# Performance work log

Hardware: AMD Instinct MI355X
Metric: run time of the kernel (lower is better)

Reference implementation:

```python
import jax, jax.numpy as jnp
import numpy as np

ROLE_BITS = 20
NHEAD = 16
D_MODEL = 1024
D_KEY = D_MODEL // NHEAD  # 64
D_FIL = 512
DFF = 4096
EPS = 1e-5


def _ln(x, g, b):
    mu = jnp.mean(x, axis=-1, keepdims=True)
    var = jnp.mean(jnp.square(x - mu), axis=-1, keepdims=True)
    return (x - mu) * jax.lax.rsqrt(var + EPS) * g + b


def setup_inputs() -> dict:
    key = jax.random.key(0)
    ks = jax.random.split(key, 10)
    N, BSZ, MEM = 16384, 16, 8
    D_IN = D_FIL + ROLE_BITS  # 532
    values = jax.random.normal(ks[0], (N, D_FIL), jnp.float32)
    role_index = jax.random.randint(ks[1], (N,), 1, 2 ** ROLE_BITS)
    # every (batch, memory_slot) pair occupied -> static shapes (compression is a no-op)
    slot = jax.random.permutation(ks[2], jnp.tile(jnp.arange(BSZ * MEM), N // (BSZ * MEM)))
    batch_index = (slot // MEM).astype(jnp.int32)
    memory_index = (slot % MEM).astype(jnp.int32)
    query_vectors = jax.random.normal(ks[3], (NHEAD, D_KEY), jnp.float32) * (1.0 / np.sqrt(D_KEY))
    s = 0.02
    Wk = jax.random.normal(ks[4], (D_MODEL, D_IN), jnp.float32) * s
    Wv = jax.random.normal(ks[5], (D_MODEL, D_IN), jnp.float32) * s
    Wo = jax.random.normal(ks[6], (D_MODEL, D_MODEL), jnp.float32) * s
    W1 = jax.random.normal(ks[7], (DFF, D_MODEL), jnp.float32) * s
    W2 = jax.random.normal(ks[8], (D_MODEL, DFF), jnp.float32) * s
    return dict(
        values=values, role_index=role_index, batch_index=batch_index,
        memory_index=memory_index, query_vectors=query_vectors,
        Wk=Wk, Wv=Wv, Wo=Wo, bo=jnp.zeros((D_MODEL,), jnp.float32),
        W1=W1, b1=jnp.zeros((DFF,), jnp.float32),
        W2=W2, b2=jnp.zeros((D_MODEL,), jnp.float32),
        g_fil=jnp.ones((D_FIL,), jnp.float32), b_fil=jnp.zeros((D_FIL,), jnp.float32),
        g_mha=jnp.ones((D_IN,), jnp.float32), b_mha=jnp.zeros((D_IN,), jnp.float32),
        g_ff=jnp.ones((D_MODEL,), jnp.float32), b_ff=jnp.zeros((D_MODEL,), jnp.float32),
        g_out=jnp.ones((D_MODEL,), jnp.float32), b_out=jnp.zeros((D_MODEL,), jnp.float32),
        bsz=BSZ, memory_slots=MEM,
    )


def _tree_positional_encodings(role_index):
    # bit-expand role indices: column j is bit j of the role index
    bits = (jnp.bitwise_and(role_index[:, None], 2 ** jnp.arange(ROLE_BITS)) != 0).astype(jnp.float32)
    # locate the highest set bit (torch: flip + argmax)
    mi = jnp.argmax(bits[:, ::-1], axis=1)
    cm = ROLE_BITS - 1 - mi  # index of highest set bit
    bits = bits * (1.0 - jax.nn.one_hot(cm, ROLE_BITS, dtype=bits.dtype))  # zero it out
    branch = jnp.arange(ROLE_BITS)[None, :] < cm[:, None]
    return jnp.where(branch, (bits - 0.5) * 2.0, bits)  # {0,1} -> {-1,1} below MSB


def reference(values, role_index, batch_index, memory_index, query_vectors,
              Wk, Wv, Wo, bo, W1, b1, W2, b2,
              g_fil, b_fil, g_mha, b_mha, g_ff, b_ff, g_out, b_out,
              bsz, memory_slots):
    N = values.shape[0]
    T = bsz * memory_slots  # num_trees (all (batch, slot) pairs occupied)

    tpd = _tree_positional_encodings(role_index)
    x = jnp.concatenate([_ln(values, g_fil, b_fil), tpd], axis=1)  # [N, d_input]
    x = _ln(x, g_mha, b_mha)
    k = (x @ Wk.T).reshape(N, NHEAD, D_KEY)
    v = (x @ Wv.T).reshape(N, NHEAD, D_KEY)
    qkm = jnp.einsum('nhd,hd->nh', k, query_vectors)  # [N, H]

    # combined batch+memory mask: node n attends to flat tree t = b*mem + m
    node_slot = batch_index * memory_slots + memory_index  # [N]
    mask = node_slot[:, None] == jnp.arange(T)[None, :]  # [N, T]
    scores = jnp.where(mask[:, :, None], qkm[:, None, :], -1e9) / np.sqrt(D_KEY)
    attn = jax.nn.softmax(scores, axis=0)  # softmax over nodes, [N, T, H]
    out = jnp.einsum('nhv,nth->thv', v, attn).reshape(T, D_MODEL)

    # post-attention: proj_o + residual with flattened queries, LN, FF, LN
    r1 = (out @ Wo.T + bo) + query_vectors.reshape(-1)
    l1 = _ln(r1, g_ff, b_ff)
    ff = jax.nn.gelu(l1 @ W1.T + b1, approximate=False) @ W2.T + b2
    l2 = _ln(ff + r1, g_out, b_out)

    rectangle_out = l2.reshape(bsz, memory_slots, D_MODEL)
    agent_pad_mask = jnp.zeros((bsz, memory_slots), dtype=bool)
    return rectangle_out, agent_pad_mask
```

## Files before the change

kernel.cpp:

```cpp
#include <hip/hip_runtime.h>
#include <hip/hip_bf16.h>

typedef __hip_bfloat16 bf16;

#define N_NODES 16384
#define D_FIL 512
#define D_IN 532
#define D_MODEL 1024
#define NHEAD 16
#define D_KEY 64
#define DFF 4096
#define NTREE 128
#define MEM_SLOTS 8
#define NODES_PER_TREE 128
#define EPS 1e-5f
#define XSE 544
#define XSU 272
#define CSTR 32
#define BSTR 40

typedef float f32x4 __attribute__((ext_vector_type(4)));
typedef short s16x8 __attribute__((ext_vector_type(8)));

union PackU { uint4 u; s16x8 s; };

__device__ inline float gelu_exact(float x) {
    return 0.5f * x * (1.0f + erff(x * 0.7071067811865476f));
}

__device__ inline void blockReduceSum2_512(float& a, float& b, float* sm) {
    int tid = threadIdx.x;
    int lane = tid & 63, wid = tid >> 6;
#pragma unroll
    for (int off = 32; off > 0; off >>= 1) {
        a += __shfl_down(a, off, 64);
        b += __shfl_down(b, off, 64);
    }
    if (lane == 0) { sm[wid] = a; sm[8 + wid] = b; }
    __syncthreads();
    if (tid == 0) {
        float s0 = 0.f, s1 = 0.f;
#pragma unroll
        for (int i = 0; i < 8; ++i) { s0 += sm[i]; s1 += sm[8 + i]; }
        sm[16] = s0; sm[17] = s1;
    }
    __syncthreads();
    a = sm[16]; b = sm[17];
}

__global__ __launch_bounds__(256) void prep_kernel(
        const float* __restrict__ values, const int* __restrict__ role,
        const int* __restrict__ bidx, const int* __restrict__ midx,
        const float* __restrict__ g_fil, const float* __restrict__ b_fil,
        const float* __restrict__ g_mha, const float* __restrict__ b_mha,
        bf16* __restrict__ xs, int* __restrict__ counts,
        const float* __restrict__ q, const float* __restrict__ Wk,
        unsigned* __restrict__ wqb,
        const float* __restrict__ Wv, float* __restrict__ wvt) {
    int b = blockIdx.x;
    int tid = threadIdx.x;

    if (b < 16) {
        int h = b;
        __shared__ float qs[64];
        if (tid < 64) qs[tid] = q[h * 64 + tid];
        __syncthreads();
        for (int p = tid; p < XSU; p += 256) {
            unsigned out = 0u;
            if (p < 266) {
                float a0 = 0.f, a1 = 0.f;
                int j0 = 2 * p;
#pragma unroll 8
                for (int d = 0; d < 64; ++d) {
                    const float* wr = Wk + (size_t)(h * 64 + d) * D_IN;
                    a0 += qs[d] * wr[j0];
                    a1 += qs[d] * wr[j0 + 1];
                }
                unsigned u0 = (unsigned)__bfloat16_as_ushort(__float2bfloat16(a0));
                unsigned u1 = (unsigned)__bfloat16_as_ushort(__float2bfloat16(a1));
                out = (u1 << 16) | u0;
            }
            wqb[h * XSU + p] = out;
        }
        return;
    }

    if (b < 560) {
        __shared__ float tile[32][33];
        int vb = b - 16;
        int c0 = (vb & 31) * 32, j0 = (vb >> 5) * 32;
        int tx = tid & 31, ty = tid >> 5;
#pragma unroll
        for (int r = 0; r < 4; ++r) {
            int cc = ty + r * 8;
            int j = j0 + tx;
            tile[cc][tx] = (j < D_IN) ? Wv[(size_t)(c0 + cc) * D_IN + j] : 0.f;
        }
        __syncthreads();
#pragma unroll
        for (int r = 0; r < 4; ++r) {
            int j = j0 + ty + r * 8;
            if (j < D_IN) wvt[(size_t)j * D_MODEL + c0 + tx] = tile[tx][ty + r * 8];
        }
        return;
    }

    int wave = tid >> 6;
    int l = tid & 63;
    int n = (b - 560) * 4 + wave;

    const float4* vp = (const float4*)(values + (size_t)n * D_FIL + l * 8);
    float4 v0 = vp[0], v1 = vp[1];

    int row = 0;
    if (l == 0) {
        int slot = bidx[n] * MEM_SLOTS + midx[n];
        int pos = atomicAdd(&counts[slot * CSTR], 1);
        row = slot * NODES_PER_TREE + pos;
    }

    float s = v0.x + v0.y + v0.z + v0.w + v1.x + v1.y + v1.z + v1.w;
    float ss = v0.x * v0.x + v0.y * v0.y + v0.z * v0.z + v0.w * v0.w
             + v1.x * v1.x + v1.y * v1.y + v1.z * v1.z + v1.w * v1.w;
#pragma unroll
    for (int m = 1; m < 64; m <<= 1) {
        s += __shfl_xor(s, m, 64);
        ss += __shfl_xor(ss, m, 64);
    }
    float mu = s * (1.f / D_FIL);
    float var = ss * (1.f / D_FIL) - mu * mu;
    float rs = rsqrtf(var + EPS);

    const float4* gf = (const float4*)(g_fil + l * 8);
    const float4* bf = (const float4*)(b_fil + l * 8);
    float4 gf0 = gf[0], gf1 = gf[1], bf0 = bf[0], bf1 = bf[1];
    float y[8];
    y[0] = (v0.x - mu) * rs * gf0.x + bf0.x;
    y[1] = (v0.y - mu) * rs * gf0.y + bf0.y;
    y[2] = (v0.z - mu) * rs * gf0.z + bf0.z;
    y[3] = (v0.w - mu) * rs * gf0.w + bf0.w;
    y[4] = (v1.x - mu) * rs * gf1.x + bf1.x;
    y[5] = (v1.y - mu) * rs * gf1.y + bf1.y;
    y[6] = (v1.z - mu) * rs * gf1.z + bf1.z;
    y[7] = (v1.w - mu) * rs * gf1.w + bf1.w;

    int r = role[n];
    int cm = 31 - __clz(r);
    float s_t = 2.f * (float)(__popc(r) - 1) - (float)cm;
    float ss_t = (float)cm;

    float s2 = y[0] + y[1] + y[2] + y[3] + y[4] + y[5] + y[6] + y[7];
    float ss2 = y[0] * y[0] + y[1] * y[1] + y[2] * y[2] + y[3] * y[3]
              + y[4] * y[4] + y[5] * y[5] + y[6] * y[6] + y[7] * y[7];
#pragma unroll
    for (int m = 1; m < 64; m <<= 1) {
        s2 += __shfl_xor(s2, m, 64);
        ss2 += __shfl_xor(ss2, m, 64);
    }
    s2 += s_t; ss2 += ss_t;
    float mu2 = s2 * (1.f / D_IN);
    float var2 = ss2 * (1.f / D_IN) - mu2 * mu2;
    float rs2 = rsqrtf(var2 + EPS);

    const float4* gm = (const float4*)(g_mha + l * 8);
    const float4* bm = (const float4*)(b_mha + l * 8);
    float4 gm0 = gm[0], gm1 = gm[1], bm0 = bm[0], bm1 = bm[1];
    float x[8];
    x[0] = (y[0] - mu2) * rs2 * gm0.x + bm0.x;
    x[1] = (y[1] - mu2) * rs2 * gm0.y + bm0.y;
    x[2] = (y[2] - mu2) * rs2 * gm0.z + bm0.z;
    x[3] = (y[3] - mu2) * rs2 * gm0.w + bm0.w;
    x[4] = (y[4] - mu2) * rs2 * gm1.x + bm1.x;
    x[5] = (y[5] - mu2) * rs2 * gm1.y + bm1.y;
    x[6] = (y[6] - mu2) * rs2 * gm1.z + bm1.z;
    x[7] = (y[7] - mu2) * rs2 * gm1.w + bm1.w;

    row = __shfl(row, 0, 64);

    {
        unsigned us[8];
#pragma unroll
        for (int k = 0; k < 8; ++k)
            us[k] = (unsigned)__bfloat16_as_ushort(__float2bfloat16(x[k]));
        uint4 pk = make_uint4((us[1] << 16) | us[0], (us[3] << 16) | us[2],
                              (us[5] << 16) | us[4], (us[7] << 16) | us[6]);
        *(uint4*)((char*)xs + (size_t)row * (XSE * 2) + 16 * l) = pk;
    }

    if (l < 20) {
        int bit = (r >> l) & 1;
        float tpd = (l < cm) ? (bit ? 1.f : -1.f) : 0.f;
        float x2 = (tpd - mu2) * rs2 * g_mha[512 + l] + b_mha[512 + l];
        xs[(size_t)row * XSE + 512 + l] = __float2bfloat16(x2);
    } else if (l < 26) {
        ((unsigned*)xs)[(size_t)row * XSU + 266 + (l - 20)] = 0u;
    }
}

__global__ __launch_bounds__(256) void qkm_kernel(const unsigned* __restrict__ xsu,
                                                  const unsigned* __restrict__ wqb,
                                                  float* __restrict__ qkmp) {
    __shared__ unsigned wshw[16 * 274];
    int tid = threadIdx.x;
#pragma unroll
    for (int hh = 0; hh < 16; ++hh) {
        wshw[hh * 274 + tid] = wqb[hh * XSU + tid];
        if (tid < 16) wshw[hh * 274 + 256 + tid] = wqb[hh * XSU + 256 + tid];
    }
    __syncthreads();

    int h = tid & 15, rp = tid >> 4;
    int r0 = blockIdx.x * 32;
    const uint2* xr0 = (const uint2*)(xsu + (size_t)(r0 + 2 * rp) * XSU);
    const uint2* xr1 = (const uint2*)(xsu + (size_t)(r0 + 2 * rp + 1) * XSU);
    const uint2* wr  = (const uint2*)(wshw + h * 274);
    float a0 = 0.f, a1 = 0.f;
#pragma unroll 8
    for (int j = 0; j < 136; ++j) {
        uint2 wu = wr[j];
        uint2 xa = xr0[j];
        uint2 xb = xr1[j];
        float w0 = __uint_as_float(wu.x << 16), w1 = __uint_as_float(wu.x & 0xffff0000u);
        float w2 = __uint_as_float(wu.y << 16), w3 = __uint_as_float(wu.y & 0xffff0000u);
        a0 += __uint_as_float(xa.x << 16) * w0 + __uint_as_float(xa.x & 0xffff0000u) * w1
            + __uint_as_float(xa.y << 16) * w2 + __uint_as_float(xa.y & 0xffff0000u) * w3;
        a1 += __uint_as_float(xb.x << 16) * w0 + __uint_as_float(xb.x & 0xffff0000u) * w1
            + __uint_as_float(xb.y << 16) * w2 + __uint_as_float(xb.y & 0xffff0000u) * w3;
    }
    qkmp[(size_t)(r0 + 2 * rp) * NHEAD + h] = a0;
    qkmp[(size_t)(r0 + 2 * rp + 1) * NHEAD + h] = a1;
}

__global__ void attn_fused_kernel(const float* __restrict__ qkmp, const unsigned* __restrict__ xsu,
                                  const float* __restrict__ wvt, float* __restrict__ attn_out) {
    int hg = blockIdx.x, t = blockIdx.y, tid = threadIdx.x;
    __shared__ __align__(16) float a4[NODES_PER_TREE * 4];
    __shared__ float zs[4][536];

    for (int l = tid; l < NODES_PER_TREE * 4; l += 256) {
        int i = l >> 2, hh = l & 3;
        a4[l] = qkmp[(size_t)t * NODES_PER_TREE * NHEAD + i * 16 + hg * 4 + hh] * 0.125f;
    }
    __syncthreads();

    int hh = tid >> 6, lane = tid & 63;
    {
        float s0 = a4[lane * 4 + hh], s1 = a4[(lane + 64) * 4 + hh];
        float m = fmaxf(s0, s1);
#pragma unroll
        for (int off = 32; off > 0; off >>= 1) m = fmaxf(m, __shfl_xor(m, off, 64));
        float e0 = expf(s0 - m), e1 = expf(s1 - m);
        float sum = e0 + e1;
#pragma unroll
        for (int off = 32; off > 0; off >>= 1) sum += __shfl_xor(sum, off, 64);
        float inv = 1.0f / sum;
        a4[lane * 4 + hh] = e0 * inv;
        a4[(lane + 64) * 4 + hh] = e1 * inv;
    }
    __syncthreads();

    {
        bool hasT = tid < 10;
        float az[4][2] = {};
        float at[4][2] = {};
        const unsigned* xt = xsu + (size_t)t * NODES_PER_TREE * XSU;
        for (int i0 = 0; i0 < NODES_PER_TREE; i0 += 8) {
            unsigned u[8], u2[8];
            float4 av[8];
#pragma unroll
            for (int k = 0; k < 8; ++k) u[k] = xt[(size_t)(i0 + k) * XSU + tid];
#pragma unroll
            for (int k = 0; k < 8; ++k) u2[k] = hasT ? xt[(size_t)(i0 + k) * XSU + 256 + tid] : 0u;
#pragma unroll
            for (int k = 0; k < 8; ++k) av[k] = *(const float4*)(a4 + (i0 + k) * 4);
#pragma unroll
            for (int k = 0; k < 8; ++k) {
                float x0 = __uint_as_float(u[k] << 16);
                float x1 = __uint_as_float(u[k] & 0xffff0000u);
                float x2 = __uint_as_float(u2[k] << 16);
                float x3 = __uint_as_float(u2[k] & 0xffff0000u);
                float4 a = av[k];
                az[0][0] += a.x * x0; az[0][1] += a.x * x1;
                az[1][0] += a.y * x0; az[1][1] += a.y * x1;
                az[2][0] += a.z * x0; az[2][1] += a.z * x1;
                az[3][0] += a.w * x0; az[3][1] += a.w * x1;
                at[0][0] += a.x * x2; at[0][1] += a.x * x3;
                at[1][0] += a.y * x2; at[1][1] += a.y * x3;
                at[2][0] += a.z * x2; at[2][1] += a.z * x3;
                at[3][0] += a.w * x2; at[3][1] += a.w * x3;
            }
        }
#pragma unroll
        for (int k = 0; k < 4; ++k) {
            *(float2*)(&zs[k][2 * tid]) = make_float2(az[k][0], az[k][1]);
            if (hasT) *(float2*)(&zs[k][512 + 2 * tid]) = make_float2(at[k][0], at[k][1]);
        }
    }
    __syncthreads();

    int c = hg * 256 + tid;
    const float* wp = wvt + c;
    float acc0 = 0.f, acc1 = 0.f;
    for (int j0 = 0; j0 < 528; j0 += 8) {
        float wv[8];
#pragma unroll
        for (int k = 0; k < 8; ++k) wv[k] = wp[(size_t)(j0 + k) * D_MODEL];
#pragma unroll
        for (int k = 0; k < 8; k += 2) {
            acc0 += zs[hh][j0 + k] * wv[k];
            acc1 += zs[hh][j0 + k + 1] * wv[k + 1];
        }
    }
    {
        float wv[4];
#pragma unroll
        for (int k = 0; k < 4; ++k) wv[k] = wp[(size_t)(528 + k) * D_MODEL];
#pragma unroll
        for (int k = 0; k < 4; k += 2) {
            acc0 += zs[hh][528 + k] * wv[k];
            acc1 += zs[hh][528 + k + 1] * wv[k + 1];
        }
    }
    attn_out[(size_t)t * D_MODEL + c] = acc0 + acc1;
}

__global__ __launch_bounds__(256) void gemm_mfma_sk(const float* __restrict__ A,
                                                    const float* __restrict__ B,
                                                    float* __restrict__ Cpart,
                                                    int N, int K, int nsb) {
    __shared__ __align__(16) unsigned short bhi[32 * BSTR];
    __shared__ __align__(16) unsigned short blo[32 * BSTR];
    int tid = threadIdx.x;
    int col0 = blockIdx.x * 32;
    int k0 = blockIdx.y * nsb * 32;
    float* C = Cpart + (size_t)blockIdx.y * 128 * N;

    int w = tid >> 6, l = tid & 63;
    int l15 = l & 15, l4 = l >> 4;
    int scol = tid >> 3, sk4 = (tid & 7) * 4;

    f32x4 acc[2][2];
#pragma unroll
    for (int rt = 0; rt < 2; ++rt)
#pragma unroll
        for (int ct = 0; ct < 2; ++ct) acc[rt][ct] = (f32x4){0.f, 0.f, 0.f, 0.f};

    for (int s = 0; s < nsb; ++s) {
        int kb = k0 + s * 32;

        const float* bp = B + (size_t)(col0 + scol) * K + kb + sk4;
        float4 fb = *(const float4*)bp;

        float4 fa[2][2];
#pragma unroll
        for (int rt = 0; rt < 2; ++rt) {
            const float* ap = A + (size_t)(32 * w + 16 * rt + l15) * K + kb + l4 * 8;
            fa[rt][0] = *(const float4*)ap;
            fa[rt][1] = *(const float4*)(ap + 4);
        }

        {
            float fe[4] = {fb.x, fb.y, fb.z, fb.w};
            unsigned hu[2], lu[2];
#pragma unroll
            for (int p = 0; p < 2; ++p) {
                unsigned u0 = __float_as_uint(fe[2 * p]);
                unsigned u1 = __float_as_uint(fe[2 * p + 1]);
                unsigned h0 = u0 & 0xffff0000u, h1 = u1 & 0xffff0000u;
                float d0 = fe[2 * p] - __uint_as_float(h0);
                float d1 = fe[2 * p + 1] - __uint_as_float(h1);
                hu[p] = h1 | (u0 >> 16);
                lu[p] = (__float_as_uint(d1) & 0xffff0000u) | (__float_as_uint(d0) >> 16);
            }
            *(uint2*)(&bhi[scol * BSTR + sk4]) = make_uint2(hu[0], hu[1]);
            *(uint2*)(&blo[scol * BSTR + sk4]) = make_uint2(lu[0], lu[1]);
        }
        __syncthreads();

        s16x8 ah[2], al[2];
#pragma unroll
        for (int rt = 0; rt < 2; ++rt) {
            float fe[8] = {fa[rt][0].x, fa[rt][0].y, fa[rt][0].z, fa[rt][0].w,
                           fa[rt][1].x, fa[rt][1].y, fa[rt][1].z, fa[rt][1].w};
            unsigned hu[4], lu[4];
#pragma unroll
            for (int p = 0; p < 4; ++p) {
                unsigned u0 = __float_as_uint(fe[2 * p]);
                unsigned u1 = __float_as_uint(fe[2 * p + 1]);
                unsigned h0 = u0 & 0xffff0000u, h1 = u1 & 0xffff0000u;
                float d0 = fe[2 * p] - __uint_as_float(h0);
                float d1 = fe[2 * p + 1] - __uint_as_float(h1);
                hu[p] = h1 | (u0 >> 16);
                lu[p] = (__float_as_uint(d1) & 0xffff0000u) | (__float_as_uint(d0) >> 16);
            }
            PackU uh, ul;
            uh.u = make_uint4(hu[0], hu[1], hu[2], hu[3]);
            ul.u = make_uint4(lu[0], lu[1], lu[2], lu[3]);
            ah[rt] = uh.s;
            al[rt] = ul.s;
        }

#pragma unroll
        for (int ct = 0; ct < 2; ++ct) {
            PackU rbh, rbl;
            rbh.u = *(const uint4*)(&bhi[(16 * ct + l15) * BSTR + l4 * 8]);
            rbl.u = *(const uint4*)(&blo[(16 * ct + l15) * BSTR + l4 * 8]);
#pragma unroll
            for (int rt = 0; rt < 2; ++rt) {
                acc[rt][ct] = __builtin_amdgcn_mfma_f32_16x16x32_bf16(ah[rt], rbh.s, acc[rt][ct], 0, 0, 0);
                acc[rt][ct] = __builtin_amdgcn_mfma_f32_16x16x32_bf16(al[rt], rbh.s, acc[rt][ct], 0, 0, 0);
                acc[rt][ct] = __builtin_amdgcn_mfma_f32_16x16x32_bf16(ah[rt], rbl.s, acc[rt][ct], 0, 0, 0);
            }
        }
        __syncthreads();
    }

#pragma unroll
    for (int rt = 0; rt < 2; ++rt) {
        int row = 32 * w + 16 * rt + l4 * 4;
#pragma unroll
        for (int ct = 0; ct < 2; ++ct) {
            int col = col0 + 16 * ct + l15;
#pragma unroll
            for (int r = 0; r < 4; ++r)
                C[(size_t)(row + r) * N + col] = acc[rt][ct][r];
        }
    }
}

__global__ __launch_bounds__(512) void ln_r1_kernel(const float* __restrict__ po, const float* __restrict__ bo,
                             const float* __restrict__ qvec, const float* __restrict__ g,
                             const float* __restrict__ b, float* __restrict__ r1,
                             float* __restrict__ l1) {
    int t = blockIdx.x, tid = threadIdx.x;
    __shared__ float sm[18];
    float e[2];
#pragma unroll
    for (int c = 0; c < 2; ++c) {
        int j = c * 512 + tid;
        float v = bo[j] + qvec[j];
#pragma unroll
        for (int s = 0; s < 8; ++s)
            v += po[(size_t)s * NTREE * D_MODEL + (size_t)t * D_MODEL + j];
        e[c] = v;
        r1[(size_t)t * D_MODEL + j] = v;
    }
    float s = e[0] + e[1];
    float ss = e[0] * e[0] + e[1] * e[1];
    blockReduceSum2_512(s, ss, sm);
    float mu = s * (1.f / D_MODEL);
    float var = ss * (1.f / D_MODEL) - mu * mu;
    float rs = rsqrtf(var + EPS);
#pragma unroll
    for (int c = 0; c < 2; ++c) {
        int j = c * 512 + tid;
        l1[(size_t)t * D_MODEL + j] = (e[c] - mu) * rs * g[j] + b[j];
    }
}

__global__ void gelu_reduce_kernel(const float* __restrict__ p1, const float* __restrict__ b1,
                                   float* __restrict__ h1) {
    int idx4 = (blockIdx.x * 256 + threadIdx.x) * 4;
    int col = idx4 & (DFF - 1);
    float4 v = *(const float4*)(b1 + col);
#pragma unroll
    for (int s = 0; s < 4; ++s) {
        float4 p = *(const float4*)(p1 + (size_t)s * NTREE * DFF + idx4);
        v.x += p.x; v.y += p.y; v.z += p.z; v.w += p.w;
    }
    v.x = gelu_exact(v.x); v.y = gelu_exact(v.y);
    v.z = gelu_exact(v.z); v.w = gelu_exact(v.w);
    *(float4*)(h1 + idx4) = v;
}

__global__ __launch_bounds__(512) void ln_out_kernel(const float* __restrict__ p2, const float* __restrict__ b2,
                              const float* __restrict__ r1, const float* __restrict__ g,
                              const float* __restrict__ b, float* __restrict__ out) {
    int t = blockIdx.x, tid = threadIdx.x;
    __shared__ float sm[18];
    float e[2];
#pragma unroll
    for (int c = 0; c < 2; ++c) {
        int j = c * 512 + tid;
        float v = b2[j] + r1[(size_t)t * D_MODEL + j];
#pragma unroll
        for (int s = 0; s < 16; ++s)
            v += p2[(size_t)s * NTREE * D_MODEL + (size_t)t * D_MODEL + j];
        e[c] = v;
    }
    float s = e[0] + e[1];
    float ss = e[0] * e[0] + e[1] * e[1];
    blockReduceSum2_512(s, ss, sm);
    float mu = s * (1.f / D_MODEL);
    float var = ss * (1.f / D_MODEL) - mu * mu;
    float rs = rsqrtf(var + EPS);
#pragma unroll
    for (int c = 0; c < 2; ++c) {
        int j = c * 512 + tid;
        out[(size_t)t * D_MODEL + j] = (e[c] - mu) * rs * g[j] + b[j];
    }
    if (t == 0 && tid < 128) out[(size_t)NTREE * D_MODEL + tid] = 0.f;
}

extern "C" void kernel_launch(void* const* d_in, const int* in_sizes, int n_in,
                              void* d_out, int out_size, void* d_ws, size_t ws_size,
                              hipStream_t stream) {
    const float* values = (const float*)d_in[0];
    const int* role     = (const int*)d_in[1];
    const int* bidx     = (const int*)d_in[2];
    const int* midx     = (const int*)d_in[3];
    const float* qvec   = (const float*)d_in[4];
    const float* Wk     = (const float*)d_in[5];
    const float* Wv     = (const float*)d_in[6];
    const float* Wo     = (const float*)d_in[7];
    const float* bo     = (const float*)d_in[8];
    const float* W1     = (const float*)d_in[9];
    const float* b1     = (const float*)d_in[10];
    const float* W2     = (const float*)d_in[11];
    const float* b2     = (const float*)d_in[12];
    const float* g_fil  = (const float*)d_in[13];
    const float* b_fil  = (const float*)d_in[14];
    const float* g_mha  = (const float*)d_in[15];
    const float* b_mha  = (const float*)d_in[16];
    const float* g_ff   = (const float*)d_in[17];
    const float* b_ff   = (const float*)d_in[18];
    const float* g_out  = (const float*)d_in[19];
    const float* b_out  = (const float*)d_in[20];

    char* w = (char*)d_ws;
    unsigned* wqb   = (unsigned*)(w + 0);
    float* qkmp     = (float*)(w + 18432);
    float* attn_out = (float*)(w + 1068032);
    float* r1       = (float*)(w + 1592320);
    float* l1       = (float*)(w + 2116608);
    float* h1       = (float*)(w + 2640896);
    int*   counts   = (int*)  (w + 2640896);
    float* wvt      = (float*)(w + 4738048);
    char*  big      = w + 6917120;
    bf16*  xs = (bf16*)big;
    float* po = (float*)big;
    float* p1 = (float*)(big + 4194304);
    float* p2 = (float*)big;

    float* out = (float*)d_out;

    hipMemsetAsync(counts, 0, 128 * CSTR * sizeof(int), stream);

    prep_kernel<<<4656, 256, 0, stream>>>(values, role, bidx, midx,
                                          g_fil, b_fil, g_mha, b_mha,
                                          xs, counts,
                                          qvec, Wk, wqb, Wv, wvt);

    qkm_kernel<<<N_NODES / 32, 256, 0, stream>>>((const unsigned*)xs, wqb, qkmp);

    attn_fused_kernel<<<dim3(4, NTREE), 256, 0, stream>>>(qkmp, (const unsigned*)xs, wvt, attn_out);

    gemm_mfma_sk<<<dim3(32, 8), 256, 0, stream>>>(attn_out, Wo, po, D_MODEL, D_MODEL, 4);

    ln_r1_kernel<<<NTREE, 512, 0, stream>>>(po, bo, qvec, g_ff, b_ff, r1, l1);

    gemm_mfma_sk<<<dim3(128, 4), 256, 0, stream>>>(l1, W1, p1, DFF, D_MODEL, 8);

    gelu_reduce_kernel<<<512, 256, 0, stream>>>(p1, b1, h1);

    gemm_mfma_sk<<<dim3(32, 16), 256, 0, stream>>>(h1, W2, p2, D_MODEL, DFF, 8);

    ln_out_kernel<<<NTREE, 512, 0, stream>>>(p2, b2, r1, g_out, b_out, out);
}
```

Measured before the change: 240.6 us.

## Fuse query-key score computation into the attention kernel

Removes the separate qkm kernel and computes the per-node head scores inside the attention kernel, for the four heads and 128 nodes each block handles. Shared memory is reused between the query-weight tile and the z staging buffer, which needs an extra barrier. This drops one launch and the qkmp round trip through global memory. In exchange each tree's node rows are read once per head-group block, and the dot loop shortens to 133 iterations, relying on the padding being zero.

```diff
diff --git a/kernel.cpp b/kernel.cpp
--- a/kernel.cpp
+++ b/kernel.cpp
@@ -197,49 +197,42 @@
     }
 }
 
-__global__ __launch_bounds__(256) void qkm_kernel(const unsigned* __restrict__ xsu,
-                                                  const unsigned* __restrict__ wqb,
-                                                  float* __restrict__ qkmp) {
-    __shared__ unsigned wshw[16 * 274];
-    int tid = threadIdx.x;
-#pragma unroll
-    for (int hh = 0; hh < 16; ++hh) {
-        wshw[hh * 274 + tid] = wqb[hh * XSU + tid];
-        if (tid < 16) wshw[hh * 274 + 256 + tid] = wqb[hh * XSU + 256 + tid];
-    }
-    __syncthreads();
-
-    int h = tid & 15, rp = tid >> 4;
-    int r0 = blockIdx.x * 32;
-    const uint2* xr0 = (const uint2*)(xsu + (size_t)(r0 + 2 * rp) * XSU);
-    const uint2* xr1 = (const uint2*)(xsu + (size_t)(r0 + 2 * rp + 1) * XSU);
-    const uint2* wr  = (const uint2*)(wshw + h * 274);
-    float a0 = 0.f, a1 = 0.f;
-#pragma unroll 8
-    for (int j = 0; j < 136; ++j) {
-        uint2 wu = wr[j];
-        uint2 xa = xr0[j];
-        uint2 xb = xr1[j];
-        float w0 = __uint_as_float(wu.x << 16), w1 = __uint_as_float(wu.x & 0xffff0000u);
-        float w2 = __uint_as_float(wu.y << 16), w3 = __uint_as_float(wu.y & 0xffff0000u);
-        a0 += __uint_as_float(xa.x << 16) * w0 + __uint_as_float(xa.x & 0xffff0000u) * w1
-            + __uint_as_float(xa.y << 16) * w2 + __uint_as_float(xa.y & 0xffff0000u) * w3;
-        a1 += __uint_as_float(xb.x << 16) * w0 + __uint_as_float(xb.x & 0xffff0000u) * w1
-            + __uint_as_float(xb.y << 16) * w2 + __uint_as_float(xb.y & 0xffff0000u) * w3;
-    }
-    qkmp[(size_t)(r0 + 2 * rp) * NHEAD + h] = a0;
-    qkmp[(size_t)(r0 + 2 * rp + 1) * NHEAD + h] = a1;
-}
-
-__global__ void attn_fused_kernel(const float* __restrict__ qkmp, const unsigned* __restrict__ xsu,
-                                  const float* __restrict__ wvt, float* __restrict__ attn_out) {
+__global__ __launch_bounds__(256) void attn_fused_kernel(const unsigned* __restrict__ xsu,
+                                                         const unsigned* __restrict__ wqb,
+                                                         const float* __restrict__ wvt,
+                                                         float* __restrict__ attn_out) {
     int hg = blockIdx.x, t = blockIdx.y, tid = threadIdx.x;
     __shared__ __align__(16) float a4[NODES_PER_TREE * 4];
-    __shared__ float zs[4][536];
-
-    for (int l = tid; l < NODES_PER_TREE * 4; l += 256) {
-        int i = l >> 2, hh = l & 3;
-        a4[l] = qkmp[(size_t)t * NODES_PER_TREE * NHEAD + i * 16 + hg * 4 + hh] * 0.125f;
+    __shared__ __align__(16) char sbuf[8576];
+    unsigned* wsh = (unsigned*)sbuf;
+    float (*zs)[536] = (float(*)[536])sbuf;
+
+    for (int i = tid; i < 4 * 274; i += 256) {
+        int hh = i / 274, p = i - hh * 274;
+        wsh[hh * 274 + p] = (p < XSU) ? wqb[(hg * 4 + hh) * XSU + p] : 0u;
+    }
+    __syncthreads();
+
+    {
+        int i = tid >> 2, hh = tid & 3;
+        const uint2* xr0 = (const uint2*)(xsu + (size_t)(t * NODES_PER_TREE + i) * XSU);
+        const uint2* xr1 = (const uint2*)(xsu + (size_t)(t * NODES_PER_TREE + i + 64) * XSU);
+        const uint2* wr  = (const uint2*)(wsh + hh * 274);
+        float a0 = 0.f, a1 = 0.f;
+#pragma unroll 8
+        for (int j = 0; j < 133; ++j) {
+            uint2 wu = wr[j];
+            uint2 xa = xr0[j];
+            uint2 xb = xr1[j];
+            float w0 = __uint_as_float(wu.x << 16), w1 = __uint_as_float(wu.x & 0xffff0000u);
+            float w2 = __uint_as_float(wu.y << 16), w3 = __uint_as_float(wu.y & 0xffff0000u);
+            a0 += __uint_as_float(xa.x << 16) * w0 + __uint_as_float(xa.x & 0xffff0000u) * w1
+                + __uint_as_float(xa.y << 16) * w2 + __uint_as_float(xa.y & 0xffff0000u) * w3;
+            a1 += __uint_as_float(xb.x << 16) * w0 + __uint_as_float(xb.x & 0xffff0000u) * w1
+                + __uint_as_float(xb.y << 16) * w2 + __uint_as_float(xb.y & 0xffff0000u) * w3;
+        }
+        a4[tid] = a0 * 0.125f;
+        a4[tid + 256] = a1 * 0.125f;
     }
     __syncthreads();
 
@@ -290,6 +283,7 @@
                 at[3][0] += a.w * x2; at[3][1] += a.w * x3;
             }
         }
+        __syncthreads();
 #pragma unroll
         for (int k = 0; k < 4; ++k) {
             *(float2*)(&zs[k][2 * tid]) = make_float2(az[k][0], az[k][1]);
@@ -528,15 +522,14 @@
     const float* b_out  = (const float*)d_in[20];
 
     char* w = (char*)d_ws;
-    unsigned* wqb   = (unsigned*)(w + 0);
-    float* qkmp     = (float*)(w + 18432);
-    float* attn_out = (float*)(w + 1068032);
-    float* r1       = (float*)(w + 1592320);
-    float* l1       = (float*)(w + 2116608);
-    float* h1       = (float*)(w + 2640896);
-    int*   counts   = (int*)  (w + 2640896);
-    float* wvt      = (float*)(w + 4738048);
-    char*  big      = w + 6917120;
+    int*   counts   = (int*)(w + 0);
+    unsigned* wqb   = (unsigned*)(w + 16384);
+    float* attn_out = (float*)(w + 34816);
+    float* r1       = (float*)(w + 559104);
+    float* l1       = (float*)(w + 1083392);
+    float* h1       = (float*)(w + 1607680);
+    float* wvt      = (float*)(w + 3704832);
+    char*  big      = w + 5883904;
     bf16*  xs = (bf16*)big;
     float* po = (float*)big;
     float* p1 = (float*)(big + 4194304);
@@ -544,16 +537,14 @@
 
     float* out = (float*)d_out;
 
-    hipMemsetAsync(counts, 0, 128 * CSTR * sizeof(int), stream);
+    hipMemsetAsync(counts, 0, 16384, stream);
 
     prep_kernel<<<4656, 256, 0, stream>>>(values, role, bidx, midx,
                                           g_fil, b_fil, g_mha, b_mha,
                                           xs, counts,
                                           qvec, Wk, wqb, Wv, wvt);
 
-    qkm_kernel<<<N_NODES / 32, 256, 0, stream>>>((const unsigned*)xs, wqb, qkmp);
-
-    attn_fused_kernel<<<dim3(4, NTREE), 256, 0, stream>>>(qkmp, (const unsigned*)xs, wvt, attn_out);
+    attn_fused_kernel<<<dim3(4, NTREE), 256, 0, stream>>>((const unsigned*)xs, wqb, wvt, attn_out);
 
     gemm_mfma_sk<<<dim3(32, 8), 256, 0, stream>>>(attn_out, Wo, po, D_MODEL, D_MODEL, 4);
 
```

New measurement: 236.6 us. Within noise of the previous version (-1.7%).
